# Kernel optimization log

Measured on AMD Instinct MI355X. Metric: run time of the kernel, lower is better.

Reference implementation:

```python
import jax, jax.numpy as jnp
import numpy as np
from jax import lax


def _pairwise_dist(a, b):
    # a: (T, D), b: (T, D) -> (T, T) Euclidean distances via GEMM trick
    a2 = jnp.sum(a * a, axis=-1)
    b2 = jnp.sum(b * b, axis=-1)
    sq = a2[:, None] + b2[None, :] - 2.0 * (a @ b.T)
    return jnp.sqrt(jnp.maximum(sq, 1e-12))


def _frechet(seq1, seq2):
    cost = _pairwise_dist(seq1, seq2)  # (T, T)
    ca0 = lax.cummax(cost[0])          # first row boundary: running max

    def row_step(prev, cost_row):
        # prev: ca[i-1, :]; cost_row: cost[i, :]
        c0 = jnp.maximum(prev[0], cost_row[0])  # first-column boundary

        def col_step(left, x):
            c, up, diag = x
            val = jnp.maximum(c, jnp.minimum(jnp.minimum(up, left), diag))
            return val, val

        _, rest = lax.scan(col_step, c0, (cost_row[1:], prev[1:], prev[:-1]))
        cur = jnp.concatenate([c0[None], rest])
        return cur, None

    final_row, _ = lax.scan(row_step, ca0, cost[1:])
    return final_row[-1]


def setup_inputs() -> dict:
    key = jax.random.key(0)
    k1, k2 = jax.random.split(key)
    B, T, D = 32, 1024, 64
    pred = jax.random.normal(k1, (B, T, D), dtype=jnp.float32)
    targ = jax.random.normal(k2, (B, T, D), dtype=jnp.float32)
    return {"pred": pred, "targ": targ}


def reference(pred, targ):
    dists = jax.vmap(_frechet)(pred, targ)  # (B,)
    return jnp.mean(dists)
```

## Files before the change

### kernel.cpp

```cpp
#include <hip/hip_runtime.h>
#include <hip/hip_bf16.h>

#define T_LEN 1024
#define D_DIM 64
#define BATCH 32

#define BM 128
#define BN 128

__global__ __launch_bounds__(256, 2) void cost_kernel(const float* __restrict__ pred,
                                                      const float* __restrict__ targ,
                                                      float* __restrict__ cost) {
    const int b = blockIdx.z;
    const float* P = pred + (size_t)b * T_LEN * D_DIM;
    const float* Tg = targ + (size_t)b * T_LEN * D_DIM;
    float* C = cost + (size_t)b * T_LEN * T_LEN;
    const int row0 = blockIdx.y * BM;
    const int col0 = blockIdx.x * BN;

    __shared__ __align__(16) float ps[BM][D_DIM + 4];
    __shared__ __align__(16) float ts[D_DIM][BN + 4];
    __shared__ float p2[BM], t2[BN];

    const int tid = threadIdx.x;

#pragma unroll
    for (int it = 0; it < 8; ++it) {
        int f = tid + 256 * it;
        int row = f >> 4;
        int kc = f & 15;
        float4 v = *(const float4*)(P + (size_t)(row0 + row) * D_DIM + 4 * kc);
        *(float4*)&ps[row][4 * kc] = v;
    }
#pragma unroll
    for (int it = 0; it < 8; ++it) {
        int f = tid + 256 * it;
        int col = f >> 4;
        int kc = f & 15;
        float4 w = *(const float4*)(Tg + (size_t)(col0 + col) * D_DIM + 4 * kc);
        ts[4 * kc + 0][col] = w.x;
        ts[4 * kc + 1][col] = w.y;
        ts[4 * kc + 2][col] = w.z;
        ts[4 * kc + 3][col] = w.w;
    }
    __syncthreads();

    if (tid < 128) {
        float s = 0.0f;
        const float4* pr = (const float4*)&ps[tid][0];
#pragma unroll
        for (int q = 0; q < 16; ++q) {
            float4 v = pr[q];
            s += v.x * v.x; s += v.y * v.y; s += v.z * v.z; s += v.w * v.w;
        }
        p2[tid] = s;
    } else {
        int c = tid - 128;
        float s = 0.0f;
#pragma unroll
        for (int k = 0; k < 64; ++k) { float x = ts[k][c]; s += x * x; }
        t2[c] = s;
    }
    __syncthreads();

    const int tx = tid & 15;
    const int ty = tid >> 4;
    const int cl = 4 * tx;
    const int ch = 64 + 4 * tx;

    float acc[8][8];
#pragma unroll
    for (int i = 0; i < 8; ++i)
#pragma unroll
        for (int j = 0; j < 8; ++j) acc[i][j] = 0.0f;

#pragma unroll
    for (int k4 = 0; k4 < 16; ++k4) {
        float4 bl[4], bh[4];
#pragma unroll
        for (int kk = 0; kk < 4; ++kk) {
            bl[kk] = *(const float4*)&ts[4 * k4 + kk][cl];
            bh[kk] = *(const float4*)&ts[4 * k4 + kk][ch];
        }
#pragma unroll
        for (int ih = 0; ih < 2; ++ih) {
#pragma unroll
            for (int i = 0; i < 4; ++i) {
                const int rr = (ih ? 64 + 4 * ty : 4 * ty) + i;
                float4 av = *(const float4*)&ps[rr][4 * k4];
                const float a4[4] = {av.x, av.y, av.z, av.w};
                float* A = acc[4 * ih + i];
#pragma unroll
                for (int kk = 0; kk < 4; ++kk) {
                    const float* blp = (const float*)&bl[kk];
                    const float* bhp = (const float*)&bh[kk];
                    const float ak = a4[kk];
#pragma unroll
                    for (int j = 0; j < 4; ++j) {
                        A[j]     += ak * blp[j];
                        A[4 + j] += ak * bhp[j];
                    }
                }
            }
        }
    }

    float4 tlo = *(const float4*)&t2[cl];
    float4 thi = *(const float4*)&t2[ch];
    const float* tl = (const float*)&tlo;
    const float* th = (const float*)&thi;
#pragma unroll
    for (int ih = 0; ih < 2; ++ih) {
#pragma unroll
        for (int i = 0; i < 4; ++i) {
            const int rr = (ih ? 64 + 4 * ty : 4 * ty) + i;
            const float pa = p2[rr];
            float* A = acc[4 * ih + i];
            float4 o1, o2;
            o1.x = sqrtf(fmaxf(pa + tl[0] - 2.0f * A[0], 1e-12f));
            o1.y = sqrtf(fmaxf(pa + tl[1] - 2.0f * A[1], 1e-12f));
            o1.z = sqrtf(fmaxf(pa + tl[2] - 2.0f * A[2], 1e-12f));
            o1.w = sqrtf(fmaxf(pa + tl[3] - 2.0f * A[3], 1e-12f));
            o2.x = sqrtf(fmaxf(pa + th[0] - 2.0f * A[4], 1e-12f));
            o2.y = sqrtf(fmaxf(pa + th[1] - 2.0f * A[5], 1e-12f));
            o2.z = sqrtf(fmaxf(pa + th[2] - 2.0f * A[6], 1e-12f));
            o2.w = sqrtf(fmaxf(pa + th[3] - 2.0f * A[7], 1e-12f));
            float* Crow = C + (size_t)(row0 + rr) * T_LEN + col0;
            *(float4*)(Crow + cl) = o1;
            *(float4*)(Crow + ch) = o2;
        }
    }
}

#define PD 8

#define DP_LOAD4(D0, D1, D2, D3, SRC)                                         \
    asm volatile("global_load_dwordx4 %0, %4, off\n\t"                        \
                 "global_load_dwordx4 %1, %4, off offset:16\n\t"              \
                 "global_load_dwordx4 %2, %4, off offset:32\n\t"              \
                 "global_load_dwordx4 %3, %4, off offset:48"                  \
                 : "=&v"(D0), "=&v"(D1), "=&v"(D2), "=&v"(D3)                 \
                 : "v"(SRC))

__global__ __launch_bounds__(64, 1) void dp_kernel(const float* __restrict__ cost,
                                                   float* __restrict__ out) {
    const int b = blockIdx.x;
    const int t = threadIdx.x;
    const float INF = __builtin_inff();
    const float* C = cost + (size_t)b * T_LEN * T_LEN + 16 * t;

    float prev[16];
#pragma unroll
    for (int j = 0; j < 16; ++j) prev[j] = INF;
    float right_out = INF;
    float diag_feed = INF;

    float4 A0, A1, A2, A3, B0, B1, B2, B3, C0_, C1_, C2_, C3_, D0_, D1_, D2_, D3_;
    float4 E0, E1, E2, E3, F0, F1, F2, F3, G0, G1, G2, G3, H0, H1, H2, H3;

#define DP_PROLOG(D, P0, P1, P2, P3)                                          \
    {                                                                         \
        int r = (D) - t; r = r < 0 ? 0 : r;                                   \
        const float* src = C + (size_t)r * T_LEN;                             \
        DP_LOAD4(P0, P1, P2, P3, src);                                        \
    }
    DP_PROLOG(0, A0, A1, A2, A3)
    DP_PROLOG(1, B0, B1, B2, B3)
    DP_PROLOG(2, C0_, C1_, C2_, C3_)
    DP_PROLOG(3, D0_, D1_, D2_, D3_)
    DP_PROLOG(4, E0, E1, E2, E3)
    DP_PROLOG(5, F0, F1, F2, F3)
    DP_PROLOG(6, G0, G1, G2, G3)
    DP_PROLOG(7, H0, H1, H2, H3)
#undef DP_PROLOG

    const int S = T_LEN + 63;
    const int NCH = (S + PD - 1) / PD;
    int s = 0;

#define DP_STEP(P0, P1, P2, P3)                                               \
    {                                                                         \
        float inc = __shfl_up(right_out, 1, 64);                              \
        asm volatile("s_waitcnt vmcnt(28)" ::: "memory");                     \
        __builtin_amdgcn_sched_barrier(0);                                    \
        const int r = s - t;                                                  \
        float left = inc, diag = diag_feed;                                   \
        diag_feed = inc;                                                      \
        if (t == 0) { left = (r == 0) ? -INF : INF; diag = INF; }             \
        if (r >= 0 && r < T_LEN) {                                            \
            float cq[16] = {P0.x, P0.y, P0.z, P0.w, P1.x, P1.y, P1.z, P1.w,   \
                            P2.x, P2.y, P2.z, P2.w, P3.x, P3.y, P3.z, P3.w};  \
            float g[16];                                                      \
            g[0] = fmaxf(cq[0], fminf(prev[0], diag));                        \
            _Pragma("unroll")                                                 \
            for (int j = 1; j < 16; ++j)                                      \
                g[j] = fmaxf(cq[j], fminf(prev[j], prev[j - 1]));             \
            float v = left;                                                   \
            _Pragma("unroll")                                                 \
            for (int j = 0; j < 16; ++j) {                                    \
                v = __builtin_amdgcn_fmed3f(v, cq[j], g[j]);                  \
                prev[j] = v;                                                  \
            }                                                                 \
            right_out = v;                                                    \
        }                                                                     \
        __builtin_amdgcn_sched_barrier(0);                                    \
        {                                                                     \
            int rn = s + PD - t;                                              \
            rn = rn < 0 ? 0 : (rn > T_LEN - 1 ? T_LEN - 1 : rn);              \
            const float* src = C + (size_t)rn * T_LEN;                        \
            DP_LOAD4(P0, P1, P2, P3, src);                                    \
        }                                                                     \
        ++s;                                                                  \
    }

    for (int chunk = 0; chunk < NCH; ++chunk) {
        DP_STEP(A0, A1, A2, A3)
        DP_STEP(B0, B1, B2, B3)
        DP_STEP(C0_, C1_, C2_, C3_)
        DP_STEP(D0_, D1_, D2_, D3_)
        DP_STEP(E0, E1, E2, E3)
        DP_STEP(F0, F1, F2, F3)
        DP_STEP(G0, G1, G2, G3)
        DP_STEP(H0, H1, H2, H3)
    }
#undef DP_STEP

    asm volatile("s_waitcnt vmcnt(0)" ::: "memory");
    if (t == 63) atomicAdd(out, prev[15] * (1.0f / (float)BATCH));
}

__global__ __launch_bounds__(64) void dp_fused_kernel(const float* __restrict__ pred,
                                                      const float* __restrict__ targ,
                                                      float* __restrict__ out) {
    const int b = blockIdx.x;
    const int t = threadIdx.x;
    const float INF = __builtin_inff();
    const float* P = pred + (size_t)b * T_LEN * D_DIM;
    const float* T = targ + (size_t)b * T_LEN * D_DIM + (size_t)(16 * t) * D_DIM;

    float prev[16];
#pragma unroll
    for (int j = 0; j < 16; ++j) prev[j] = INF;
    float right_out = INF;
    float diag_feed = INF;

    for (int s = 0; s < T_LEN + 63; s++) {
        int r = s - t;
        float inc = __shfl_up(right_out, 1, 64);
        float left = inc, diag = diag_feed;
        diag_feed = inc;
        if (t == 0) { left = (r == 0) ? -INF : INF; diag = INF; }
        if (r >= 0 && r < T_LEN) {
            float4 pr[16];
            const float4* pp = (const float4*)(P + (size_t)r * D_DIM);
#pragma unroll
            for (int q = 0; q < 16; q++) pr[q] = pp[q];
#pragma unroll
            for (int j = 0; j < 16; j++) {
                const float4* tp = (const float4*)(T + (size_t)j * D_DIM);
                float acc = 0.0f;
#pragma unroll
                for (int q = 0; q < 16; q++) {
                    float4 tv = tp[q];
                    float dx = pr[q].x - tv.x; acc += dx * dx;
                    float dy = pr[q].y - tv.y; acc += dy * dy;
                    float dz = pr[q].z - tv.z; acc += dz * dz;
                    float dw = pr[q].w - tv.w; acc += dw * dw;
                }
                float c = sqrtf(fmaxf(acc, 1e-12f));
                float up = prev[j];
                float v = fmaxf(c, fminf(fminf(up, diag), left));
                diag = up; left = v; prev[j] = v;
            }
            right_out = left;
        }
    }
    if (t == 63) atomicAdd(out, prev[15] * (1.0f / (float)BATCH));
}

extern "C" void kernel_launch(void* const* d_in, const int* in_sizes, int n_in,
                              void* d_out, int out_size, void* d_ws, size_t ws_size,
                              hipStream_t stream) {
    const float* pred = (const float*)d_in[0];
    const float* targ = (const float*)d_in[1];
    float* out = (float*)d_out;

    hipMemsetAsync(out, 0, sizeof(float) * out_size, stream);

    const size_t per_batch = (size_t)T_LEN * T_LEN * sizeof(float);
    int bpg = (int)(ws_size / per_batch);
    if (bpg > BATCH) bpg = BATCH;

    if (bpg >= 1) {
        float* cost = (float*)d_ws;
        for (int g0 = 0; g0 < BATCH; g0 += bpg) {
            int gb = (BATCH - g0) < bpg ? (BATCH - g0) : bpg;
            dim3 grid(T_LEN / BN, T_LEN / BM, gb);
            cost_kernel<<<grid, 256, 0, stream>>>(pred + (size_t)g0 * T_LEN * D_DIM,
                                                  targ + (size_t)g0 * T_LEN * D_DIM,
                                                  cost);
            dp_kernel<<<gb, 64, 0, stream>>>(cost, out);
        }
    } else {
        dp_fused_kernel<<<BATCH, 64, 0, stream>>>(pred, targ, out);
    }
}
```

Measured before the change: 367.7 us.

## Process two DP rows per wavefront step and use compiler-scheduled loads

The anti-diagonal DP kernel now advances two rows of the cost matrix per step, so it needs about half as many sequential wavefront steps and lane shuffles. The hand-written global loads with explicit vmcnt waits are replaced by plain float4 loads prefetched a few steps ahead. This targets the sequential latency of the wavefront. It risks worse overlap of memory and compute, because the compiler chooses where to wait, and it raises register pressure.

Result: slower. 376.7 us (+2.4%).

```diff
diff --git a/kernel.cpp b/kernel.cpp
--- a/kernel.cpp
+++ b/kernel.cpp
@@ -132,15 +132,7 @@
     }
 }
 
-#define PD 8
-
-#define DP_LOAD4(D0, D1, D2, D3, SRC)                                         \
-    asm volatile("global_load_dwordx4 %0, %4, off\n\t"                        \
-                 "global_load_dwordx4 %1, %4, off offset:16\n\t"              \
-                 "global_load_dwordx4 %2, %4, off offset:32\n\t"              \
-                 "global_load_dwordx4 %3, %4, off offset:48"                  \
-                 : "=&v"(D0), "=&v"(D1), "=&v"(D2), "=&v"(D3)                 \
-                 : "v"(SRC))
+#define PD2 4
 
 __global__ __launch_bounds__(64, 1) void dp_kernel(const float* __restrict__ cost,
                                                    float* __restrict__ out) {
@@ -152,80 +144,98 @@
     float prev[16];
 #pragma unroll
     for (int j = 0; j < 16; ++j) prev[j] = INF;
-    float right_out = INF;
-    float diag_feed = INF;
-
-    float4 A0, A1, A2, A3, B0, B1, B2, B3, C0_, C1_, C2_, C3_, D0_, D1_, D2_, D3_;
-    float4 E0, E1, E2, E3, F0, F1, F2, F3, G0, G1, G2, G3, H0, H1, H2, H3;
-
-#define DP_PROLOG(D, P0, P1, P2, P3)                                          \
+    float right0 = INF;
+    float right1 = INF;
+    float diag2 = INF;
+
+    float4 s0a0, s0a1, s0a2, s0a3, s0b0, s0b1, s0b2, s0b3;
+    float4 s1a0, s1a1, s1a2, s1a3, s1b0, s1b1, s1b2, s1b3;
+    float4 s2a0, s2a1, s2a2, s2a3, s2b0, s2b1, s2b2, s2b3;
+    float4 s3a0, s3a1, s3a2, s3a3, s3b0, s3b1, s3b2, s3b3;
+
+#define DP2_FILL(D, A0, A1, A2, A3, B0, B1, B2, B3)                           \
     {                                                                         \
-        int r = (D) - t; r = r < 0 ? 0 : r;                                   \
-        const float* src = C + (size_t)r * T_LEN;                             \
-        DP_LOAD4(P0, P1, P2, P3, src);                                        \
-    }
-    DP_PROLOG(0, A0, A1, A2, A3)
-    DP_PROLOG(1, B0, B1, B2, B3)
-    DP_PROLOG(2, C0_, C1_, C2_, C3_)
-    DP_PROLOG(3, D0_, D1_, D2_, D3_)
-    DP_PROLOG(4, E0, E1, E2, E3)
-    DP_PROLOG(5, F0, F1, F2, F3)
-    DP_PROLOG(6, G0, G1, G2, G3)
-    DP_PROLOG(7, H0, H1, H2, H3)
-#undef DP_PROLOG
-
-    const int S = T_LEN + 63;
-    const int NCH = (S + PD - 1) / PD;
+        int rn = 2 * ((D) - t);                                               \
+        rn = rn < 0 ? 0 : (rn > T_LEN - 2 ? T_LEN - 2 : rn);                  \
+        const float4* p0 = (const float4*)(C + (size_t)rn * T_LEN);           \
+        const float4* p1 = (const float4*)(C + (size_t)(rn + 1) * T_LEN);     \
+        A0 = p0[0]; A1 = p0[1]; A2 = p0[2]; A3 = p0[3];                       \
+        B0 = p1[0]; B1 = p1[1]; B2 = p1[2]; B3 = p1[3];                       \
+    }
+    DP2_FILL(0, s0a0, s0a1, s0a2, s0a3, s0b0, s0b1, s0b2, s0b3)
+    DP2_FILL(1, s1a0, s1a1, s1a2, s1a3, s1b0, s1b1, s1b2, s1b3)
+    DP2_FILL(2, s2a0, s2a1, s2a2, s2a3, s2b0, s2b1, s2b2, s2b3)
+    DP2_FILL(3, s3a0, s3a1, s3a2, s3a3, s3b0, s3b1, s3b2, s3b3)
+#undef DP2_FILL
+
+    const int S2 = (T_LEN / 2) + 63;
+    const int NCH = (S2 + PD2 - 1) / PD2;
     int s = 0;
 
-#define DP_STEP(P0, P1, P2, P3)                                               \
+#define DP2_STEP(A0, A1, A2, A3, B0, B1, B2, B3)                              \
     {                                                                         \
-        float inc = __shfl_up(right_out, 1, 64);                              \
-        asm volatile("s_waitcnt vmcnt(28)" ::: "memory");                     \
-        __builtin_amdgcn_sched_barrier(0);                                    \
-        const int r = s - t;                                                  \
-        float left = inc, diag = diag_feed;                                   \
-        diag_feed = inc;                                                      \
-        if (t == 0) { left = (r == 0) ? -INF : INF; diag = INF; }             \
-        if (r >= 0 && r < T_LEN) {                                            \
-            float cq[16] = {P0.x, P0.y, P0.z, P0.w, P1.x, P1.y, P1.z, P1.w,   \
-                            P2.x, P2.y, P2.z, P2.w, P3.x, P3.y, P3.z, P3.w};  \
+           \
+        float4 a0 = A0, a1 = A1, a2 = A2, a3 = A3;                            \
+        float4 b0 = B0, b1 = B1, b2 = B2, b3 = B3;                            \
+        {                                                                     \
+            int rn = 2 * (s + PD2 - t);                                       \
+            rn = rn < 0 ? 0 : (rn > T_LEN - 2 ? T_LEN - 2 : rn);              \
+            const float4* p0 = (const float4*)(C + (size_t)rn * T_LEN);       \
+            const float4* p1 = (const float4*)(C + (size_t)(rn + 1) * T_LEN); \
+            A0 = p0[0]; A1 = p0[1]; A2 = p0[2]; A3 = p0[3];                   \
+            B0 = p1[0]; B1 = p1[1]; B2 = p1[2]; B3 = p1[3];                   \
+        }                                                                     \
+        const int r0 = 2 * (s - t);                                           \
+        float inc0 = __shfl_up(right0, 1, 64);                                \
+        float inc1 = __shfl_up(right1, 1, 64);                                \
+        float left0 = inc0, diag0 = diag2;                                    \
+        float left1 = inc1, diag1 = inc0;                                     \
+        diag2 = inc1;                                                         \
+        if (t == 0) {                                                         \
+            left0 = (r0 == 0) ? -INF : INF;                                   \
+            diag0 = INF; left1 = INF; diag1 = INF;                            \
+        }                                                                     \
+        if (r0 >= 0 && r0 < T_LEN) {                                          \
+            float ca[16] = {a0.x, a0.y, a0.z, a0.w, a1.x, a1.y, a1.z, a1.w,   \
+                            a2.x, a2.y, a2.z, a2.w, a3.x, a3.y, a3.z, a3.w};  \
+            float cb[16] = {b0.x, b0.y, b0.z, b0.w, b1.x, b1.y, b1.z, b1.w,   \
+                            b2.x, b2.y, b2.z, b2.w, b3.x, b3.y, b3.z, b3.w};  \
             float g[16];                                                      \
-            g[0] = fmaxf(cq[0], fminf(prev[0], diag));                        \
+            g[0] = fmaxf(ca[0], fminf(prev[0], diag0));                       \
             _Pragma("unroll")                                                 \
             for (int j = 1; j < 16; ++j)                                      \
-                g[j] = fmaxf(cq[j], fminf(prev[j], prev[j - 1]));             \
-            float v = left;                                                   \
+                g[j] = fmaxf(ca[j], fminf(prev[j], prev[j - 1]));             \
+            float v = left0;                                                  \
             _Pragma("unroll")                                                 \
             for (int j = 0; j < 16; ++j) {                                    \
-                v = __builtin_amdgcn_fmed3f(v, cq[j], g[j]);                  \
+                v = __builtin_amdgcn_fmed3f(v, ca[j], g[j]);                  \
                 prev[j] = v;                                                  \
             }                                                                 \
-            right_out = v;                                                    \
-        }                                                                     \
-        __builtin_amdgcn_sched_barrier(0);                                    \
-        {                                                                     \
-            int rn = s + PD - t;                                              \
-            rn = rn < 0 ? 0 : (rn > T_LEN - 1 ? T_LEN - 1 : rn);              \
-            const float* src = C + (size_t)rn * T_LEN;                        \
-            DP_LOAD4(P0, P1, P2, P3, src);                                    \
+            right0 = v;                                                       \
+            float h[16];                                                      \
+            h[0] = fmaxf(cb[0], fminf(prev[0], diag1));                       \
+            _Pragma("unroll")                                                 \
+            for (int j = 1; j < 16; ++j)                                      \
+                h[j] = fmaxf(cb[j], fminf(prev[j], prev[j - 1]));             \
+            float w = left1;                                                  \
+            _Pragma("unroll")                                                 \
+            for (int j = 0; j < 16; ++j) {                                    \
+                w = __builtin_amdgcn_fmed3f(w, cb[j], h[j]);                  \
+                prev[j] = w;                                                  \
+            }                                                                 \
+            right1 = w;                                                       \
         }                                                                     \
         ++s;                                                                  \
     }
 
     for (int chunk = 0; chunk < NCH; ++chunk) {
-        DP_STEP(A0, A1, A2, A3)
-        DP_STEP(B0, B1, B2, B3)
-        DP_STEP(C0_, C1_, C2_, C3_)
-        DP_STEP(D0_, D1_, D2_, D3_)
-        DP_STEP(E0, E1, E2, E3)
-        DP_STEP(F0, F1, F2, F3)
-        DP_STEP(G0, G1, G2, G3)
-        DP_STEP(H0, H1, H2, H3)
-    }
-#undef DP_STEP
-
-    asm volatile("s_waitcnt vmcnt(0)" ::: "memory");
+        DP2_STEP(s0a0, s0a1, s0a2, s0a3, s0b0, s0b1, s0b2, s0b3)
+        DP2_STEP(s1a0, s1a1, s1a2, s1a3, s1b0, s1b1, s1b2, s1b3)
+        DP2_STEP(s2a0, s2a1, s2a2, s2a3, s2b0, s2b1, s2b2, s2b3)
+        DP2_STEP(s3a0, s3a1, s3a2, s3a3, s3b0, s3b1, s3b2, s3b3)
+    }
+#undef DP2_STEP
+
     if (t == 63) atomicAdd(out, prev[15] * (1.0f / (float)BATCH));
 }
 
```
